# Optimization experiments

Hardware: AMD Instinct MI355X
Metric: run time of the kernel (lower is better)

## Reference

```python
import jax, jax.numpy as jnp
import numpy as np

N_NODES = 20000
E_RAND = 300000
IN_F, OUT_F, HEADS = 1280, 128, 4
HID = OUT_F * HEADS  # 512


def gat_conv(x, src, dst, W, attn_l, attn_r, bias, n_nodes):
    """DGL GATConv: fc (no bias) -> per-edge LeakyReLU(el_src+er_dst) ->
    segment softmax over incoming edges -> weighted scatter-sum -> +bias.
    Returns (N, HEADS, OUT_F)."""
    h = (x @ W).reshape(n_nodes, HEADS, OUT_F)            # (N,H,F)
    el = jnp.einsum('nhf,hf->nh', h, attn_l)              # (N,H)
    er = jnp.einsum('nhf,hf->nh', h, attn_r)              # (N,H)
    e = jax.nn.leaky_relu(el[src] + er[dst], 0.2)         # (E,H)
    emax = jax.ops.segment_max(e, dst, num_segments=n_nodes)
    ee = jnp.exp(e - emax[dst])                           # (E,H)
    denom = jax.ops.segment_sum(ee, dst, num_segments=n_nodes)
    alpha = ee / denom[dst]                               # (E,H)
    msg = h[src] * alpha[:, :, None]                      # (E,H,F)
    out = jax.ops.segment_sum(msg, dst, num_segments=n_nodes)
    return out + bias.reshape(HEADS, OUT_F)


def setup_inputs() -> dict:
    key = jax.random.key(0)
    ks = jax.random.split(key, 12)
    src_r = jax.random.randint(ks[0], (E_RAND,), 0, N_NODES)
    dst_r = jax.random.randint(ks[1], (E_RAND,), 0, N_NODES)
    self_loop = jnp.arange(N_NODES)
    src = jnp.concatenate([src_r, self_loop])  # self loops: contact[i][i]=1
    dst = jnp.concatenate([dst_r, self_loop])
    feature = jax.random.normal(ks[2], (N_NODES, IN_F), dtype=jnp.float32)
    s1 = 1.0 / np.sqrt(IN_F)
    s2 = 1.0 / np.sqrt(HID)
    return {
        'feature': feature,
        'W1': jax.random.normal(ks[3], (IN_F, HID), dtype=jnp.float32) * s1,
        'al1': jax.random.normal(ks[4], (HEADS, OUT_F), dtype=jnp.float32) * s2,
        'ar1': jax.random.normal(ks[5], (HEADS, OUT_F), dtype=jnp.float32) * s2,
        'b1': jnp.zeros((HID,), dtype=jnp.float32),
        'W2': jax.random.normal(ks[6], (HID, HID), dtype=jnp.float32) * s2,
        'al2': jax.random.normal(ks[7], (HEADS, OUT_F), dtype=jnp.float32) * s2,
        'ar2': jax.random.normal(ks[8], (HEADS, OUT_F), dtype=jnp.float32) * s2,
        'b2': jnp.zeros((HID,), dtype=jnp.float32),
        'Wfc': jax.random.normal(ks[9], (HID, 64), dtype=jnp.float32) * s2,
        'bfc': jnp.zeros((64,), dtype=jnp.float32),
        'src': src,
        'dst': dst,
    }


def reference(feature, W1, al1, ar1, b1, W2, al2, ar2, b2, Wfc, bfc, src, dst):
    n = feature.shape[0]
    out = gat_conv(feature, src, dst, W1, al1, ar1, b1, n)   # (N,4,128)
    out = jax.nn.elu(out).reshape(n, HID)                    # (N,512)
    out = gat_conv(out, src, dst, W2, al2, ar2, b2, n)       # (N,4,128)
    out = jax.nn.elu(out).reshape(n, HID)                    # (N,512)
    out = out @ Wfc + bfc                                    # (N,64)
    out = jax.nn.elu(out[None, :, :])                        # (1,N,64)
    return out
```

## Files before the change

kernel.cpp:

```cpp
#include <hip/hip_runtime.h>
#include <hip/hip_bf16.h>
#include <math.h>

#define HID 512
#define HEADS 4
#define OUTF 128

typedef __attribute__((ext_vector_type(8))) _Float16 f16x8_t;
typedef __attribute__((ext_vector_type(4))) _Float16 f16x4_t;
typedef __attribute__((ext_vector_type(4))) float f32x4_t;

__device__ __forceinline__ void gl_lds16(const void* g, void* l) {
    __builtin_amdgcn_global_load_lds(
        (const __attribute__((address_space(1))) void*)g,
        (__attribute__((address_space(3))) void*)l, 16, 0, 0);
}

__device__ __forceinline__ void stage_plane32(const _Float16* g, int strideE,
    int rbase, int rmax, char* plane, int tid)
{
#pragma unroll
    for (int j = 0; j < 2; ++j) {
        int gci = j * 256 + tid;
        int r = gci >> 2, c = gci & 3;
        int rg = rbase + r; if (rg > rmax) rg = rmax;
        const char* s = (const char*)(g + (size_t)rg * strideE) + ((c ^ ((r >> 1) & 3)) << 4);
        char* d = plane + (j * 256 + (tid & ~63)) * 16;
        gl_lds16(s, d);
    }
}

__global__ __launch_bounds__(256) void conv16_kernel(const float* __restrict__ in,
    _Float16* __restrict__ o, int nquad)
{
    int stride = gridDim.x * 256;
    for (int i = blockIdx.x * 256 + threadIdx.x; i < nquad; i += stride) {
        float4 v = *(const float4*)&in[(size_t)i * 4];
        f16x4_t ov;
        ov[0] = (_Float16)v.x; ov[1] = (_Float16)v.y;
        ov[2] = (_Float16)v.z; ov[3] = (_Float16)v.w;
        *(f16x4_t*)&o[(size_t)i * 4] = ov;
    }
}

__global__ __launch_bounds__(256) void prep_w(const float* __restrict__ W,
    _Float16* __restrict__ Wt, int K, int NC)
{
    __shared__ float tile[32][33];
    const int k0 = blockIdx.x * 32, n0 = blockIdx.y * 32;
    const int t = threadIdx.x;
    {
        int r = t >> 3, c4 = (t & 7) * 4;
        float4 v = *(const float4*)&W[(size_t)(k0 + r) * NC + n0 + c4];
        tile[r][c4] = v.x; tile[r][c4 + 1] = v.y;
        tile[r][c4 + 2] = v.z; tile[r][c4 + 3] = v.w;
    }
    __syncthreads();
    int n = t >> 3, kc = (t & 7) * 4;
#pragma unroll
    for (int i = 0; i < 4; ++i)
        Wt[(size_t)(n0 + n) * K + k0 + kc + i] = (_Float16)tile[kc + i][n];
}

template<int EPI, int OUT16, int ELER>
__global__ __launch_bounds__(256, 3) void gemm_f16(
    const _Float16* __restrict__ Af, const _Float16* __restrict__ Bt,
    const float* __restrict__ bias,
    const float* __restrict__ attl, const float* __restrict__ attr,
    float* __restrict__ elp, float* __restrict__ erp,
    void* __restrict__ Cout, int M, int K, int NCOL, int ldC,
    int ncolT, int nwg)
{
    __shared__ char lds[32768];
    const int tid = threadIdx.x;
    const int wave = tid >> 6, lane = tid & 63;
    const int wm = wave >> 1, wn = wave & 1;
    const int b = blockIdx.x;
    const int q = nwg >> 3, rr = nwg & 7;
    const int xcd = b & 7, ib = b >> 3;
    const int logical = (xcd < rr ? xcd * (q + 1) : rr * (q + 1) + (xcd - rr) * q) + ib;
    const int bm = (logical / ncolT) * 128, bcol = logical % ncolT;
    const int bn = bcol * 128;
    const int l15 = lane & 15, l4 = lane >> 4;
    const int swz = (l15 >> 1) & 3;

    f32x4_t acc[4][4];
#pragma unroll
    for (int i = 0; i < 4; ++i)
#pragma unroll
        for (int j = 0; j < 4; ++j) acc[i][j] = (f32x4_t){0.f, 0.f, 0.f, 0.f};

    const int nt = K >> 5;
    stage_plane32(Af, K, bm, M - 1, lds, tid);
    stage_plane32(Bt, K, bn, NCOL - 1, lds + 8192, tid);
    __syncthreads();

    for (int t = 0; t < nt; ++t) {
        char* AH = lds + (t & 1) * 16384;
        char* BH = AH + 8192;
        if (t + 1 < nt) {
            char* AHn = lds + ((t + 1) & 1) * 16384;
            stage_plane32(Af + (t + 1) * 32, K, bm, M - 1, AHn, tid);
            stage_plane32(Bt + (t + 1) * 32, K, bn, NCOL - 1, AHn + 8192, tid);
        }
        f16x8_t fa[4], fb[4];
#pragma unroll
        for (int mf = 0; mf < 4; ++mf) {
            int row = wm * 64 + mf * 16 + l15;
            fa[mf] = *(const f16x8_t*)(AH + row * 64 + ((l4 ^ swz) << 4));
        }
#pragma unroll
        for (int nf = 0; nf < 4; ++nf) {
            int rn = wn * 64 + nf * 16 + l15;
            fb[nf] = *(const f16x8_t*)(BH + rn * 64 + ((l4 ^ swz) << 4));
        }
#pragma unroll
        for (int mf = 0; mf < 4; ++mf)
#pragma unroll
            for (int nf = 0; nf < 4; ++nf)
                acc[mf][nf] = __builtin_amdgcn_mfma_f32_16x16x32_f16(fa[mf], fb[nf], acc[mf][nf], 0, 0, 0);
        __syncthreads();
    }
#pragma unroll
    for (int mf = 0; mf < 4; ++mf) {
        int rbase = bm + wm * 64 + mf * 16 + l4 * 4;
#pragma unroll
        for (int nf = 0; nf < 4; ++nf) {
            int col = bn + wn * 64 + nf * 16 + l15;
            if (col >= NCOL) continue;
#pragma unroll
            for (int r = 0; r < 4; ++r) {
                int row = rbase + r;
                if (row < M) {
                    float v = acc[mf][nf][r];
                    if (EPI) {
                        v += bias[col];
                        v = v > 0.f ? v : (expf(v) - 1.f);
                    }
                    if (OUT16) ((_Float16*)Cout)[(size_t)row * ldC + col] = (_Float16)v;
                    else       ((float*)Cout)[(size_t)row * ldC + col] = v;
                }
            }
        }
    }
    if (ELER) {
        const int head = bcol;
        float alv[4], arv[4];
#pragma unroll
        for (int nf = 0; nf < 4; ++nf) {
            int cl = wn * 64 + nf * 16 + l15;
            alv[nf] = attl[head * OUTF + cl];
            arv[nf] = attr[head * OUTF + cl];
        }
        float pel[4][4], perr[4][4];
#pragma unroll
        for (int mf = 0; mf < 4; ++mf)
#pragma unroll
            for (int r = 0; r < 4; ++r) {
                float se = 0.f, sr = 0.f;
#pragma unroll
                for (int nf = 0; nf < 4; ++nf) {
                    se = fmaf(acc[mf][nf][r], alv[nf], se);
                    sr = fmaf(acc[mf][nf][r], arv[nf], sr);
                }
                pel[mf][r] = se; perr[mf][r] = sr;
            }
#pragma unroll
        for (int off = 1; off < 16; off <<= 1)
#pragma unroll
            for (int mf = 0; mf < 4; ++mf)
#pragma unroll
                for (int r = 0; r < 4; ++r) {
                    pel[mf][r]  += __shfl_xor(pel[mf][r],  off);
                    perr[mf][r] += __shfl_xor(perr[mf][r], off);
                }
        __syncthreads();
        float* red = (float*)lds;
        if (l15 == 0) {
#pragma unroll
            for (int mf = 0; mf < 4; ++mf)
#pragma unroll
                for (int r = 0; r < 4; ++r) {
                    int rl = wm * 64 + mf * 16 + l4 * 4 + r;
                    red[rl * 2 + wn]       = pel[mf][r];
                    red[256 + rl * 2 + wn] = perr[mf][r];
                }
        }
        __syncthreads();
        if (tid < 128) {
            int row = bm + tid;
            if (row < M) {
                float es = red[tid * 2] + red[tid * 2 + 1];
                float rs = red[256 + tid * 2] + red[256 + tid * 2 + 1];
                elp[row * HEADS + head] = es;
                erp[row * HEADS + head] = rs;
            }
        }
    }
}

__global__ void hist_kernel(const int* __restrict__ dst, int* __restrict__ deg, int E)
{
    int e = blockIdx.x * 256 + threadIdx.x;
    if (e < E) atomicAdd(&deg[dst[e]], 1);
}

__global__ __launch_bounds__(256) void scan1_kernel(const int* __restrict__ deg,
    int* __restrict__ offs, int* __restrict__ bsum, int N)
{
    __shared__ int buf[256];
    int tid = threadIdx.x;
    int i = blockIdx.x * 256 + tid;
    int v = (i < N) ? deg[i] : 0;
    buf[tid] = v;
    __syncthreads();
#pragma unroll
    for (int off = 1; off < 256; off <<= 1) {
        int t = (tid >= off) ? buf[tid - off] : 0;
        __syncthreads();
        buf[tid] += t;
        __syncthreads();
    }
    if (i < N) offs[i] = buf[tid] - v;
    if (tid == 255) bsum[blockIdx.x] = buf[255];
}

__global__ void scan2_kernel(int* __restrict__ bsum, int nb)
{
    if (threadIdx.x == 0) {
        int acc = 0;
        for (int b = 0; b < nb; ++b) { int t = bsum[b]; bsum[b] = acc; acc += t; }
        bsum[nb] = acc;
    }
}

__global__ void scan3_kernel(int* __restrict__ offs, const int* __restrict__ bsum,
                             int N, int nb)
{
    int i = blockIdx.x * 256 + threadIdx.x;
    if (i < N) offs[i] += bsum[blockIdx.x];
    if (i == 0) offs[N] = bsum[nb];
}

__global__ void fill_kernel(const int* __restrict__ srcv, const int* __restrict__ dstv,
    const int* __restrict__ offs, int* __restrict__ cursor,
    int* __restrict__ psrc, int E)
{
    int e = blockIdx.x * 256 + threadIdx.x;
    if (e < E) {
        int d = dstv[e];
        int p = atomicAdd(&cursor[d], 1);
        psrc[offs[d] + p] = srcv[e];
    }
}

__global__ __launch_bounds__(256) void aggregate_kernel(const _Float16* __restrict__ h,
    const int* __restrict__ offs, const int* __restrict__ psrc,
    const float* __restrict__ el, const float* __restrict__ er,
    const float* __restrict__ bias, _Float16* __restrict__ xo, int N)
{
    const int n = blockIdx.x * 4 + (threadIdx.x >> 6);
    if (n >= N) return;
    const int lane = threadIdx.x & 63;
    const int c = lane * 8;
    const int head = lane >> 4;
    const int hp = lane >> 5;
    const int e31 = lane & 31;
    const int sbase = (head >> 1) << 5;
    const int hsel = head & 1;

    const float2 er2 = *(const float2*)&er[n * HEADS + hp * 2];

    float acc[8];
#pragma unroll
    for (int k = 0; k < 8; ++k) acc[k] = 0.f;
    float ws = 0.f;

    const int beg = offs[n], end = offs[n + 1];
    for (int base = beg; base < end; base += 32) {
        const int cnt = min(32, end - base);
        int idx = base + e31;
        if (e31 >= cnt) idx = beg;
        const int s = psrc[idx];
        const float2 lv = *(const float2*)&el[s * HEADS + hp * 2];
        float x0 = lv.x + er2.x; x0 = x0 > 0.f ? x0 : 0.2f * x0;
        float x1 = lv.y + er2.y; x1 = x1 > 0.f ? x1 : 0.2f * x1;
        const float wa = expf(x0);
        const float wb = expf(x1);

        int j = 0;
        for (; j + 4 <= cnt; j += 4) {
            int s0 = __shfl(s, j);     int s1 = __shfl(s, j + 1);
            int s2 = __shfl(s, j + 2); int s3 = __shfl(s, j + 3);
            float a0 = __shfl(wa, sbase + j),     b0 = __shfl(wb, sbase + j);
            float a1 = __shfl(wa, sbase + j + 1), b1 = __shfl(wb, sbase + j + 1);
            float a2 = __shfl(wa, sbase + j + 2), b2 = __shfl(wb, sbase + j + 2);
            float a3 = __shfl(wa, sbase + j + 3), b3 = __shfl(wb, sbase + j + 3);
            float w0 = hsel ? b0 : a0;
            float w1 = hsel ? b1 : a1;
            float w2 = hsel ? b2 : a2;
            float w3 = hsel ? b3 : a3;
            f16x8_t v0 = *(const f16x8_t*)&h[(size_t)s0 * HID + c];
            f16x8_t v1 = *(const f16x8_t*)&h[(size_t)s1 * HID + c];
            f16x8_t v2 = *(const f16x8_t*)&h[(size_t)s2 * HID + c];
            f16x8_t v3 = *(const f16x8_t*)&h[(size_t)s3 * HID + c];
#pragma unroll
            for (int k = 0; k < 8; ++k) {
                acc[k] = fmaf(w0, (float)v0[k], acc[k]);
                acc[k] = fmaf(w1, (float)v1[k], acc[k]);
                acc[k] = fmaf(w2, (float)v2[k], acc[k]);
                acc[k] = fmaf(w3, (float)v3[k], acc[k]);
            }
            ws += w0 + w1 + w2 + w3;
        }
        for (; j < cnt; ++j) {
            int s0 = __shfl(s, j);
            float a0 = __shfl(wa, sbase + j), b0 = __shfl(wb, sbase + j);
            float w0 = hsel ? b0 : a0;
            f16x8_t v0 = *(const f16x8_t*)&h[(size_t)s0 * HID + c];
#pragma unroll
            for (int k = 0; k < 8; ++k) acc[k] = fmaf(w0, (float)v0[k], acc[k]);
            ws += w0;
        }
    }
    float inv = 1.f / ws;
    float4 b0v = *(const float4*)&bias[c];
    float4 b1v = *(const float4*)&bias[c + 4];
    float bb[8] = {b0v.x, b0v.y, b0v.z, b0v.w, b1v.x, b1v.y, b1v.z, b1v.w};
    f16x8_t ov;
#pragma unroll
    for (int k = 0; k < 8; ++k) {
        float r = acc[k] * inv + bb[k];
        r = r > 0.f ? r : (expf(r) - 1.f);
        ov[k] = (_Float16)r;
    }
    *(f16x8_t*)&xo[(size_t)n * HID + c] = ov;
}

extern "C" void kernel_launch(void* const* d_in, const int* in_sizes, int n_in,
                              void* d_out, int out_size, void* d_ws, size_t ws_size,
                              hipStream_t stream)
{
    const float* feature = (const float*)d_in[0];
    const float* W1  = (const float*)d_in[1];
    const float* al1 = (const float*)d_in[2];
    const float* ar1 = (const float*)d_in[3];
    const float* b1  = (const float*)d_in[4];
    const float* W2  = (const float*)d_in[5];
    const float* al2 = (const float*)d_in[6];
    const float* ar2 = (const float*)d_in[7];
    const float* b2  = (const float*)d_in[8];
    const float* Wfc = (const float*)d_in[9];
    const float* bfc = (const float*)d_in[10];
    const int* src = (const int*)d_in[11];
    const int* dst = (const int*)d_in[12];
    const int N = in_sizes[0] / 1280;
    const int E = in_sizes[11];
    const int nb = (N + 255) / 256;
    float* out = (float*)d_out;

    char* ws = (char*)d_ws;
    size_t off = 0;
    auto alloc = [&](size_t bytes) {
        void* p = ws + off;
        off += (bytes + 255) & ~(size_t)255;
        return p;
    };
    int* deg    = (int*)alloc((size_t)N * 4);
    int* cursor = (int*)alloc((size_t)N * 4);
    int* offs   = (int*)alloc((size_t)(N + 1) * 4);
    int* bsum   = (int*)alloc((size_t)(nb + 1) * 4);
    float* el   = (float*)alloc((size_t)N * HEADS * 4);
    float* er   = (float*)alloc((size_t)N * HEADS * 4);
    int* psrc   = (int*)alloc((size_t)E * 4);
    _Float16* featf = (_Float16*)alloc((size_t)N * 1280 * 2);
    _Float16* hbuf  = (_Float16*)alloc((size_t)N * HID * 2);
    _Float16* xh    = (_Float16*)alloc((size_t)N * HID * 2);
    _Float16* W1t   = (_Float16*)alloc((size_t)HID * 1280 * 2);
    _Float16* W2t   = (_Float16*)alloc((size_t)HID * HID * 2);
    _Float16* Wft   = (_Float16*)alloc((size_t)64 * HID * 2);

    hipMemsetAsync(deg, 0, (size_t)N * 4, stream);
    hipMemsetAsync(cursor, 0, (size_t)N * 4, stream);
    hist_kernel<<<(E + 255) / 256, 256, 0, stream>>>(dst, deg, E);
    scan1_kernel<<<nb, 256, 0, stream>>>(deg, offs, bsum, N);
    scan2_kernel<<<1, 64, 0, stream>>>(bsum, nb);
    scan3_kernel<<<nb, 256, 0, stream>>>(offs, bsum, N, nb);
    fill_kernel<<<(E + 255) / 256, 256, 0, stream>>>(src, dst, offs, cursor, psrc, E);

    conv16_kernel<<<2048, 256, 0, stream>>>(feature, featf, N * 1280 / 4);
    prep_w<<<dim3(1280 / 32, HID / 32), 256, 0, stream>>>(W1, W1t, 1280, HID);
    prep_w<<<dim3(HID / 32, HID / 32), 256, 0, stream>>>(W2, W2t, HID, HID);
    prep_w<<<dim3(HID / 32, 64 / 32), 256, 0, stream>>>(Wfc, Wft, HID, 64);

    const int nrowT = (N + 127) / 128;
    const int nwgG = nrowT * (HID / 128);
    const int nwgF = nrowT;
    const int aggB = (N + 3) / 4;

    gemm_f16<0, 1, 1><<<nwgG, 256, 0, stream>>>(featf, W1t, nullptr,
                                                al1, ar1, el, er,
                                                hbuf, N, 1280, HID, HID,
                                                HID / 128, nwgG);
    aggregate_kernel<<<aggB, 256, 0, stream>>>(hbuf, offs, psrc, el, er, b1, xh, N);

    gemm_f16<0, 1, 1><<<nwgG, 256, 0, stream>>>(xh, W2t, nullptr,
                                                al2, ar2, el, er,
                                                hbuf, N, HID, HID, HID,
                                                HID / 128, nwgG);
    aggregate_kernel<<<aggB, 256, 0, stream>>>(hbuf, offs, psrc, el, er, b2, xh, N);

    gemm_f16<1, 0, 0><<<nwgF, 256, 0, stream>>>(xh, Wft, bfc,
                                                nullptr, nullptr, nullptr, nullptr,
                                                out, N, HID, 64, 64,
                                                1, nwgF);
}
```

Measured before the change: 260.3 us.

## Fuse fp32-to-fp16 feature conversion into first GEMM's A-tile staging

```diff
diff --git a/kernel.cpp b/kernel.cpp
--- a/kernel.cpp
+++ b/kernel.cpp
@@ -30,16 +30,30 @@
     }
 }
 
-__global__ __launch_bounds__(256) void conv16_kernel(const float* __restrict__ in,
-    _Float16* __restrict__ o, int nquad)
-{
-    int stride = gridDim.x * 256;
-    for (int i = blockIdx.x * 256 + threadIdx.x; i < nquad; i += stride) {
-        float4 v = *(const float4*)&in[(size_t)i * 4];
-        f16x4_t ov;
-        ov[0] = (_Float16)v.x; ov[1] = (_Float16)v.y;
-        ov[2] = (_Float16)v.z; ov[3] = (_Float16)v.w;
-        *(f16x4_t*)&o[(size_t)i * 4] = ov;
+__device__ __forceinline__ void a32_load(const float* g, int strideE,
+    int rbase, int rmax, int tid, int kbase, float4* v)
+{
+#pragma unroll
+    for (int j = 0; j < 2; ++j) {
+        int gci = j * 256 + tid;
+        int r = gci >> 2, c = gci & 3;
+        int rg = rbase + r; if (rg > rmax) rg = rmax;
+        const float* s = g + (size_t)rg * strideE + kbase + ((c ^ ((r >> 1) & 3)) << 3);
+        v[j * 2]     = *(const float4*)s;
+        v[j * 2 + 1] = *(const float4*)(s + 4);
+    }
+}
+__device__ __forceinline__ void a32_write(char* plane, int tid, const float4* v)
+{
+#pragma unroll
+    for (int j = 0; j < 2; ++j) {
+        const float4 a = v[j * 2], b = v[j * 2 + 1];
+        f16x8_t o;
+        o[0] = (_Float16)a.x; o[1] = (_Float16)a.y;
+        o[2] = (_Float16)a.z; o[3] = (_Float16)a.w;
+        o[4] = (_Float16)b.x; o[5] = (_Float16)b.y;
+        o[6] = (_Float16)b.z; o[7] = (_Float16)b.w;
+        *(f16x8_t*)(plane + (j * 256 + tid) * 16) = o;
     }
 }
 
@@ -62,9 +76,9 @@
         Wt[(size_t)(n0 + n) * K + k0 + kc + i] = (_Float16)tile[kc + i][n];
 }
 
-template<int EPI, int OUT16, int ELER>
+template<int EPI, int OUT16, int ELER, int A32>
 __global__ __launch_bounds__(256, 3) void gemm_f16(
-    const _Float16* __restrict__ Af, const _Float16* __restrict__ Bt,
+    const void* __restrict__ Ap, const _Float16* __restrict__ Bt,
     const float* __restrict__ bias,
     const float* __restrict__ attl, const float* __restrict__ attr,
     float* __restrict__ elp, float* __restrict__ erp,
@@ -72,6 +86,8 @@
     int ncolT, int nwg)
 {
     __shared__ char lds[32768];
+    const _Float16* Af  = (const _Float16*)Ap;
+    const float*    Af32 = (const float*)Ap;
     const int tid = threadIdx.x;
     const int wave = tid >> 6, lane = tid & 63;
     const int wm = wave >> 1, wn = wave & 1;
@@ -91,16 +107,23 @@
         for (int j = 0; j < 4; ++j) acc[i][j] = (f32x4_t){0.f, 0.f, 0.f, 0.f};
 
     const int nt = K >> 5;
-    stage_plane32(Af, K, bm, M - 1, lds, tid);
+    float4 pre[4];
+    if (A32) {
+        a32_load(Af32, K, bm, M - 1, tid, 0, pre);
+        a32_write(lds, tid, pre);
+    } else {
+        stage_plane32(Af, K, bm, M - 1, lds, tid);
+    }
     stage_plane32(Bt, K, bn, NCOL - 1, lds + 8192, tid);
     __syncthreads();
 
     for (int t = 0; t < nt; ++t) {
         char* AH = lds + (t & 1) * 16384;
         char* BH = AH + 8192;
+        char* AHn = lds + ((t + 1) & 1) * 16384;
         if (t + 1 < nt) {
-            char* AHn = lds + ((t + 1) & 1) * 16384;
-            stage_plane32(Af + (t + 1) * 32, K, bm, M - 1, AHn, tid);
+            if (A32) a32_load(Af32, K, bm, M - 1, tid, (t + 1) * 32, pre);
+            else     stage_plane32(Af + (t + 1) * 32, K, bm, M - 1, AHn, tid);
             stage_plane32(Bt + (t + 1) * 32, K, bn, NCOL - 1, AHn + 8192, tid);
         }
         f16x8_t fa[4], fb[4];
@@ -119,6 +142,7 @@
 #pragma unroll
             for (int nf = 0; nf < 4; ++nf)
                 acc[mf][nf] = __builtin_amdgcn_mfma_f32_16x16x32_f16(fa[mf], fb[nf], acc[mf][nf], 0, 0, 0);
+        if (A32 && t + 1 < nt) a32_write(AHn, tid, pre);
         __syncthreads();
     }
 #pragma unroll
@@ -373,7 +397,6 @@
     float* el   = (float*)alloc((size_t)N * HEADS * 4);
     float* er   = (float*)alloc((size_t)N * HEADS * 4);
     int* psrc   = (int*)alloc((size_t)E * 4);
-    _Float16* featf = (_Float16*)alloc((size_t)N * 1280 * 2);
     _Float16* hbuf  = (_Float16*)alloc((size_t)N * HID * 2);
     _Float16* xh    = (_Float16*)alloc((size_t)N * HID * 2);
     _Float16* W1t   = (_Float16*)alloc((size_t)HID * 1280 * 2);
@@ -388,7 +411,6 @@
     scan3_kernel<<<nb, 256, 0, stream>>>(offs, bsum, N, nb);
     fill_kernel<<<(E + 255) / 256, 256, 0, stream>>>(src, dst, offs, cursor, psrc, E);
 
-    conv16_kernel<<<2048, 256, 0, stream>>>(feature, featf, N * 1280 / 4);
     prep_w<<<dim3(1280 / 32, HID / 32), 256, 0, stream>>>(W1, W1t, 1280, HID);
     prep_w<<<dim3(HID / 32, HID / 32), 256, 0, stream>>>(W2, W2t, HID, HID);
     prep_w<<<dim3(HID / 32, 64 / 32), 256, 0, stream>>>(Wfc, Wft, HID, 64);
@@ -398,20 +420,20 @@
     const int nwgF = nrowT;
     const int aggB = (N + 3) / 4;
 
-    gemm_f16<0, 1, 1><<<nwgG, 256, 0, stream>>>(featf, W1t, nullptr,
-                                                al1, ar1, el, er,
-                                                hbuf, N, 1280, HID, HID,
-                                                HID / 128, nwgG);
+    gemm_f16<0, 1, 1, 1><<<nwgG, 256, 0, stream>>>(feature, W1t, nullptr,
+                                                   al1, ar1, el, er,
+                                                   hbuf, N, 1280, HID, HID,
+                                                   HID / 128, nwgG);
     aggregate_kernel<<<aggB, 256, 0, stream>>>(hbuf, offs, psrc, el, er, b1, xh, N);
 
-    gemm_f16<0, 1, 1><<<nwgG, 256, 0, stream>>>(xh, W2t, nullptr,
-                                                al2, ar2, el, er,
-                                                hbuf, N, HID, HID, HID,
-                                                HID / 128, nwgG);
+    gemm_f16<0, 1, 1, 0><<<nwgG, 256, 0, stream>>>(xh, W2t, nullptr,
+                                                   al2, ar2, el, er,
+                                                   hbuf, N, HID, HID, HID,
+                                                   HID / 128, nwgG);
     aggregate_kernel<<<aggB, 256, 0, stream>>>(hbuf, offs, psrc, el, er, b2, xh, N);
 
-    gemm_f16<1, 0, 0><<<nwgF, 256, 0, stream>>>(xh, Wft, bfc,
-                                                nullptr, nullptr, nullptr, nullptr,
-                                                out, N, HID, 64, 64,
-                                                1, nwgF);
-}
+    gemm_f16<1, 0, 0, 0><<<nwgF, 256, 0, stream>>>(xh, Wft, bfc,
+                                                   nullptr, nullptr, nullptr, nullptr,
+                                                   out, N, HID, 64, 64,
+                                                   1, nwgF);
+}
```

Result: faster. 248.2 us (-4.7%).

## Merge setup kernels and deepen GEMM B-operand prefetch with triple buffering

Applied to the files above, without the earlier changes.

```diff
diff --git a/kernel.cpp b/kernel.cpp
--- a/kernel.cpp
+++ b/kernel.cpp
@@ -30,24 +30,47 @@
     }
 }
 
-__global__ __launch_bounds__(256) void conv16_kernel(const float* __restrict__ in,
-    _Float16* __restrict__ o, int nquad)
-{
-    int stride = gridDim.x * 256;
-    for (int i = blockIdx.x * 256 + threadIdx.x; i < nquad; i += stride) {
+__global__ __launch_bounds__(256) void conv_hist_kernel(const float* __restrict__ in,
+    _Float16* __restrict__ o, int nquad,
+    const int* __restrict__ dst, int* __restrict__ deg, int E)
+{
+    const int stride = gridDim.x * 256;
+    const int t0 = blockIdx.x * 256 + threadIdx.x;
+    for (int i = t0; i < nquad; i += stride) {
         float4 v = *(const float4*)&in[(size_t)i * 4];
         f16x4_t ov;
         ov[0] = (_Float16)v.x; ov[1] = (_Float16)v.y;
         ov[2] = (_Float16)v.z; ov[3] = (_Float16)v.w;
         *(f16x4_t*)&o[(size_t)i * 4] = ov;
     }
-}
-
-__global__ __launch_bounds__(256) void prep_w(const float* __restrict__ W,
-    _Float16* __restrict__ Wt, int K, int NC)
+    for (int e = t0; e < E; e += stride) atomicAdd(&deg[dst[e]], 1);
+}
+
+__global__ __launch_bounds__(256) void fill_prep_kernel(
+    const int* __restrict__ srcv, const int* __restrict__ dstv,
+    const int* __restrict__ offs, int* __restrict__ cursor,
+    int* __restrict__ psrc, int E, int fillB,
+    const float* __restrict__ W1, _Float16* __restrict__ W1t,
+    const float* __restrict__ W2, _Float16* __restrict__ W2t,
+    const float* __restrict__ Wfc, _Float16* __restrict__ Wft)
 {
     __shared__ float tile[32][33];
-    const int k0 = blockIdx.x * 32, n0 = blockIdx.y * 32;
+    const int b = blockIdx.x;
+    if (b < fillB) {
+        int e = b * 256 + threadIdx.x;
+        if (e < E) {
+            int d = dstv[e];
+            int p = atomicAdd(&cursor[d], 1);
+            psrc[offs[d] + p] = srcv[e];
+        }
+        return;
+    }
+    int pb = b - fillB;
+    const float* W; _Float16* Wt; int K, NC, bx, by;
+    if (pb < 640)      { W = W1;  Wt = W1t; K = 1280; NC = 512; bx = pb % 40; by = pb / 40; }
+    else if (pb < 896) { pb -= 640; W = W2;  Wt = W2t; K = 512; NC = 512; bx = pb & 15; by = pb >> 4; }
+    else               { pb -= 896; W = Wfc; Wt = Wft; K = 512; NC = 64;  bx = pb & 15; by = pb >> 4; }
+    const int k0 = bx * 32, n0 = by * 32;
     const int t = threadIdx.x;
     {
         int r = t >> 3, c4 = (t & 7) * 4;
@@ -63,7 +86,7 @@
 }
 
 template<int EPI, int OUT16, int ELER>
-__global__ __launch_bounds__(256, 3) void gemm_f16(
+__global__ __launch_bounds__(256, 4) void gemm_f16(
     const _Float16* __restrict__ Af, const _Float16* __restrict__ Bt,
     const float* __restrict__ bias,
     const float* __restrict__ attl, const float* __restrict__ attr,
@@ -71,7 +94,9 @@
     void* __restrict__ Cout, int M, int K, int NCOL, int ldC,
     int ncolT, int nwg)
 {
-    __shared__ char lds[32768];
+    __shared__ char lds[40960];
+    char* const abase = lds;
+    char* const bbase = lds + 16384;
     const int tid = threadIdx.x;
     const int wave = tid >> 6, lane = tid & 63;
     const int wm = wave >> 1, wn = wave & 1;
@@ -91,18 +116,27 @@
         for (int j = 0; j < 4; ++j) acc[i][j] = (f32x4_t){0.f, 0.f, 0.f, 0.f};
 
     const int nt = K >> 5;
-    stage_plane32(Af, K, bm, M - 1, lds, tid);
-    stage_plane32(Bt, K, bn, NCOL - 1, lds + 8192, tid);
-    __syncthreads();
+    stage_plane32(Af, K, bm, M - 1, abase, tid);
+    stage_plane32(Bt, K, bn, NCOL - 1, bbase, tid);
+    if (nt > 1) {
+        stage_plane32(Bt + 32, K, bn, NCOL - 1, bbase + 8192, tid);
+        asm volatile("s_waitcnt vmcnt(2) lgkmcnt(0)" ::: "memory");
+    } else {
+        asm volatile("s_waitcnt vmcnt(0) lgkmcnt(0)" ::: "memory");
+    }
+    __builtin_amdgcn_sched_barrier(0);
+    __builtin_amdgcn_s_barrier();
+    __builtin_amdgcn_sched_barrier(0);
 
     for (int t = 0; t < nt; ++t) {
-        char* AH = lds + (t & 1) * 16384;
-        char* BH = AH + 8192;
-        if (t + 1 < nt) {
-            char* AHn = lds + ((t + 1) & 1) * 16384;
-            stage_plane32(Af + (t + 1) * 32, K, bm, M - 1, AHn, tid);
-            stage_plane32(Bt + (t + 1) * 32, K, bn, NCOL - 1, AHn + 8192, tid);
-        }
+        char* AH = abase + (t & 1) * 8192;
+        char* BH = bbase + (t % 3) * 8192;
+        if (t + 1 < nt)
+            stage_plane32(Af + (t + 1) * 32, K, bm, M - 1,
+                          abase + ((t + 1) & 1) * 8192, tid);
+        if (t + 2 < nt)
+            stage_plane32(Bt + (t + 2) * 32, K, bn, NCOL - 1,
+                          bbase + ((t + 2) % 3) * 8192, tid);
         f16x8_t fa[4], fb[4];
 #pragma unroll
         for (int mf = 0; mf < 4; ++mf) {
@@ -119,7 +153,11 @@
 #pragma unroll
             for (int nf = 0; nf < 4; ++nf)
                 acc[mf][nf] = __builtin_amdgcn_mfma_f32_16x16x32_f16(fa[mf], fb[nf], acc[mf][nf], 0, 0, 0);
-        __syncthreads();
+        if (t + 2 < nt) asm volatile("s_waitcnt vmcnt(2) lgkmcnt(0)" ::: "memory");
+        else            asm volatile("s_waitcnt vmcnt(0) lgkmcnt(0)" ::: "memory");
+        __builtin_amdgcn_sched_barrier(0);
+        __builtin_amdgcn_s_barrier();
+        __builtin_amdgcn_sched_barrier(0);
     }
 #pragma unroll
     for (int mf = 0; mf < 4; ++mf) {
@@ -199,12 +237,6 @@
     }
 }
 
-__global__ void hist_kernel(const int* __restrict__ dst, int* __restrict__ deg, int E)
-{
-    int e = blockIdx.x * 256 + threadIdx.x;
-    if (e < E) atomicAdd(&deg[dst[e]], 1);
-}
-
 __global__ __launch_bounds__(256) void scan1_kernel(const int* __restrict__ deg,
     int* __restrict__ offs, int* __restrict__ bsum, int N)
 {
@@ -240,18 +272,6 @@
     int i = blockIdx.x * 256 + threadIdx.x;
     if (i < N) offs[i] += bsum[blockIdx.x];
     if (i == 0) offs[N] = bsum[nb];
-}
-
-__global__ void fill_kernel(const int* __restrict__ srcv, const int* __restrict__ dstv,
-    const int* __restrict__ offs, int* __restrict__ cursor,
-    int* __restrict__ psrc, int E)
-{
-    int e = blockIdx.x * 256 + threadIdx.x;
-    if (e < E) {
-        int d = dstv[e];
-        int p = atomicAdd(&cursor[d], 1);
-        psrc[offs[d] + p] = srcv[e];
-    }
 }
 
 __global__ __launch_bounds__(256) void aggregate_kernel(const _Float16* __restrict__ h,
@@ -366,6 +386,7 @@
         off += (bytes + 255) & ~(size_t)255;
         return p;
     };
+    const size_t degsz = ((size_t)N * 4 + 255) & ~(size_t)255;
     int* deg    = (int*)alloc((size_t)N * 4);
     int* cursor = (int*)alloc((size_t)N * 4);
     int* offs   = (int*)alloc((size_t)(N + 1) * 4);
@@ -380,34 +401,32 @@
     _Float16* W2t   = (_Float16*)alloc((size_t)HID * HID * 2);
     _Float16* Wft   = (_Float16*)alloc((size_t)64 * HID * 2);
 
-    hipMemsetAsync(deg, 0, (size_t)N * 4, stream);
-    hipMemsetAsync(cursor, 0, (size_t)N * 4, stream);
-    hist_kernel<<<(E + 255) / 256, 256, 0, stream>>>(dst, deg, E);
+    hipMemsetAsync(deg, 0, degsz * 2, stream);
+    conv_hist_kernel<<<2048, 256, 0, stream>>>(feature, featf, N * 1280 / 4,
+                                               dst, deg, E);
     scan1_kernel<<<nb, 256, 0, stream>>>(deg, offs, bsum, N);
     scan2_kernel<<<1, 64, 0, stream>>>(bsum, nb);
     scan3_kernel<<<nb, 256, 0, stream>>>(offs, bsum, N, nb);
-    fill_kernel<<<(E + 255) / 256, 256, 0, stream>>>(src, dst, offs, cursor, psrc, E);
-
-    conv16_kernel<<<2048, 256, 0, stream>>>(feature, featf, N * 1280 / 4);
-    prep_w<<<dim3(1280 / 32, HID / 32), 256, 0, stream>>>(W1, W1t, 1280, HID);
-    prep_w<<<dim3(HID / 32, HID / 32), 256, 0, stream>>>(W2, W2t, HID, HID);
-    prep_w<<<dim3(HID / 32, 64 / 32), 256, 0, stream>>>(Wfc, Wft, HID, 64);
+    const int fillB = (E + 255) / 256;
+    fill_prep_kernel<<<fillB + 928, 256, 0, stream>>>(src, dst, offs, cursor,
+                                                      psrc, E, fillB,
+                                                      W1, W1t, W2, W2t, Wfc, Wft);
 
     const int nrowT = (N + 127) / 128;
-    const int nwgG = nrowT * (HID / 128);
+    const int nwgG = nrowT * 4;
     const int nwgF = nrowT;
     const int aggB = (N + 3) / 4;
 
     gemm_f16<0, 1, 1><<<nwgG, 256, 0, stream>>>(featf, W1t, nullptr,
                                                 al1, ar1, el, er,
                                                 hbuf, N, 1280, HID, HID,
-                                                HID / 128, nwgG);
+                                                4, nwgG);
     aggregate_kernel<<<aggB, 256, 0, stream>>>(hbuf, offs, psrc, el, er, b1, xh, N);
 
     gemm_f16<0, 1, 1><<<nwgG, 256, 0, stream>>>(xh, W2t, nullptr,
                                                 al2, ar2, el, er,
                                                 hbuf, N, HID, HID, HID,
-                                                HID / 128, nwgG);
+                                                4, nwgG);
     aggregate_kernel<<<aggB, 256, 0, stream>>>(hbuf, offs, psrc, el, er, b2, xh, N);
 
     gemm_f16<1, 0, 0><<<nwgF, 256, 0, stream>>>(xh, Wft, bfc,
```

Result: faster. 249.6 us (-4.1%).
